# Optimization experiments

Hardware: AMD Instinct MI355X
Metric: run time of the kernel (lower is better)

## Reference

```python
import jax, jax.numpy as jnp
import numpy as np

B, N, M, K = 8, 9225, 4096, 32
D = 2          # coordinate dim
HID = 64       # MLP hidden
DOUT = 16      # MLP output / f_y channels


def setup_inputs() -> dict:
    key = jax.random.key(0)
    ks = jax.random.split(key, 10)
    y = jax.random.uniform(ks[0], (B, N, D), dtype=jnp.float32)
    x = jax.random.uniform(ks[1], (B, M, D), dtype=jnp.float32)
    f_y = jax.random.uniform(ks[2], (B, N, DOUT), dtype=jnp.float32)
    weights = jax.random.uniform(ks[3], (B, N), dtype=jnp.float32)
    neighbors_index = jax.random.randint(ks[4], (B, M, K), 0, N, dtype=jnp.int64)
    drop = jax.random.uniform(ks[5], (B, M, K)) < 0.1
    neighbors_index = jnp.where(drop, jnp.int64(-1), neighbors_index)
    # LinearChannelMLP params: 4 -> 64 -> 16, gelu between
    W1 = jax.random.normal(ks[6], (2 * D, HID), dtype=jnp.float32) * (1.0 / np.sqrt(2 * D))
    b1 = jnp.zeros((HID,), dtype=jnp.float32)
    W2 = jax.random.normal(ks[7], (HID, DOUT), dtype=jnp.float32) * (1.0 / np.sqrt(HID))
    b2 = jnp.zeros((DOUT,), dtype=jnp.float32)
    return {"y": y, "x": x, "f_y": f_y, "weights": weights,
            "W1": W1, "b1": b1, "W2": W2, "b2": b2,
            "neighbors_index": neighbors_index}


def _batched_gather(table, idx):
    # table: [B, N, ...], idx: [B, M, K] -> [B, M, K, ...]
    return jax.vmap(lambda t, i: t[i])(table, idx)


def reference(y, x, f_y, weights, W1, b1, W2, b2, neighbors_index):
    idx = jnp.where(neighbors_index == -1, 0, neighbors_index)      # [B,M,K]
    valid = (neighbors_index != -1).astype(y.dtype)[..., None]      # [B,M,K,1]

    rep_y = _batched_gather(y, idx)                                 # [B,M,K,D]
    in_f = _batched_gather(f_y, idx)                                # [B,M,K,DOUT]
    self_x = jnp.broadcast_to(x[:, :, None, :], rep_y.shape)        # [B,M,K,D]

    agg = jnp.concatenate([rep_y, self_x], axis=-1)                 # [B,M,K,2D]
    h = jax.nn.gelu(agg @ W1 + b1, approximate=False)               # [B,M,K,HID]
    kval = h @ W2 + b2                                              # [B,M,K,DOUT]

    kval = kval * in_f                                              # linear transform: k(x,y)*f(y)
    w_nbr = _batched_gather(weights, idx)[..., None]                # [B,M,K,1]
    kval = kval * w_nbr * valid
    return kval.sum(axis=2)                                         # [B,M,DOUT]
```

## Files before the change

### kernel.cpp

```cpp
#include <hip/hip_runtime.h>
#include <hip/hip_bf16.h>

#define B_    8
#define N_    9225
#define M_    4096
#define K_    32
#define HID_  64
#define DOUT_ 16

typedef __attribute__((ext_vector_type(8))) short short8;
typedef __attribute__((ext_vector_type(4))) float floatx4;
typedef __attribute__((ext_vector_type(2))) float f32x2;

static __device__ __forceinline__ short f2bf(float f) {
    __hip_bfloat16 h = __float2bfloat16(f);
    return __builtin_bit_cast(short, h);
}
static __device__ __forceinline__ f32x2 splat2(float v) { return (f32x2){v, v}; }
static __device__ __forceinline__ int bpermi(int src_bytes, int v) {
    return __builtin_amdgcn_ds_bpermute(src_bytes, v);
}
static __device__ __forceinline__ float bpermf(int src_bytes, float v) {
    return __builtin_bit_cast(float,
        __builtin_amdgcn_ds_bpermute(src_bytes, __builtin_bit_cast(int, v)));
}

static __device__ __forceinline__ float row16_sum(float v) {
    int t;
    t = __builtin_amdgcn_update_dpp(0, __builtin_bit_cast(int, v), 0x111, 0xF, 0xF, true);
    v += __builtin_bit_cast(float, t);
    t = __builtin_amdgcn_update_dpp(0, __builtin_bit_cast(int, v), 0x112, 0xF, 0xF, true);
    v += __builtin_bit_cast(float, t);
    t = __builtin_amdgcn_update_dpp(0, __builtin_bit_cast(int, v), 0x114, 0xF, 0xF, true);
    v += __builtin_bit_cast(float, t);
    t = __builtin_amdgcn_update_dpp(0, __builtin_bit_cast(int, v), 0x118, 0xF, 0xF, true);
    v += __builtin_bit_cast(float, t);
    return v;
}

static __device__ __forceinline__ f32x2 gelu2(f32x2 x) {
    const f32x2 xsq = x * x;
    const f32x2 t   = __builtin_elementwise_fma(xsq, splat2(0.035677408f), splat2(0.79788456f));
    const f32x2 z   = x * t;
    const f32x2 u   = z * z;
    const f32x2 a   = u + splat2(105.0f);
    const f32x2 nin = __builtin_elementwise_fma(u, a, splat2(945.0f));
    const f32x2 num = z * nin;
    const f32x2 bq  = __builtin_elementwise_fma(u, splat2(15.0f), splat2(420.0f));
    const f32x2 den = __builtin_elementwise_fma(u, bq, splat2(945.0f));
    const f32x2 r   = { __builtin_amdgcn_rcpf(den[0]), __builtin_amdgcn_rcpf(den[1]) };
    f32x2 th = num * r;
    th = __builtin_elementwise_min(__builtin_elementwise_max(th, splat2(-1.0f)), splat2(1.0f));
    const f32x2 hx = x * splat2(0.5f);
    return __builtin_elementwise_fma(hx, th, hx);
}

__global__ __launch_bounds__(256) void it_kernel(
    const float* __restrict__ y,
    const float* __restrict__ x,
    const float* __restrict__ f_y,
    const float* __restrict__ weights,
    const float* __restrict__ W1,
    const float* __restrict__ b1,
    const float* __restrict__ W2,
    const float* __restrict__ b2,
    const int*   __restrict__ nbr,
    float*       __restrict__ out)
{
    __shared__ float W1L[4][64];
    __shared__ float b1L[64];
    __shared__ float b2L[16];

    const int tid  = threadIdx.x;
    W1L[tid >> 6][tid & 63] = W1[tid];
    if (tid < 64) b1L[tid] = b1[tid];
    if (tid < 16) b2L[tid] = b2[tid];

    const int lane = tid & 63;
    const int q    = lane >> 4;
    const int nlo  = lane & 15;
    const int blk   = blockIdx.x;
    const int batch = blk & 7;
    const int pidx  = (blk >> 3) * 4 + (tid >> 6);
    const int row0  = __builtin_amdgcn_readfirstlane(batch * M_ + pidx * 2);
    const int bbase = batch * N_;

    const int r_g = lane >> 5, kk = lane & 31;
    const int raw = nbr[(size_t)(row0 + r_g) * K_ + kk];
    const int vld = raw >= 0;
    const int bn_g = bbase + (vld ? raw : 0);
    const float2 yvg = *(const float2*)(y + (size_t)bn_g * 2);
    const float  wg  = vld ? weights[bn_g] : 0.0f;

    short8 w2f[2];
    #pragma unroll
    for (int ch = 0; ch < 2; ++ch)
        #pragma unroll
        for (int jj = 0; jj < 8; ++jj)
            w2f[ch][jj] = f2bf(W2[(ch*32 + q*8 + jj) * DOUT_ + nlo]);

    __syncthreads();

    float partial[4] = {0.f, 0.f, 0.f, 0.f};
    #pragma unroll
    for (int ph = 0; ph < 4; ++ph) {
        const int it = ph >> 1, h = ph & 1;
        const int src = ((it << 5) + (h << 4) + nlo) << 2;

        const int bn = bpermi(src, bn_g);
        const floatx4 fv = *(const floatx4*)(f_y + (size_t)bn * 16 + q * 4);

        f32x2 yv;
        yv[0] = bpermf(src, yvg.x);
        yv[1] = bpermf(src, yvg.y);
        const float s = bpermf(src, wg);
        const float2 xv = *(const float2*)(x + (size_t)(row0 + it) * 2);

        short8 hf[2];
        #pragma unroll
        for (int ch = 0; ch < 2; ++ch) {
            #pragma unroll
            for (int p = 0; p < 4; ++p) {
                const int j = ch*32 + q*8 + 2*p;
                f32x2 hin = *(const f32x2*)&b1L[j];
                hin = __builtin_elementwise_fma(splat2(yv[0]), *(const f32x2*)&W1L[0][j], hin);
                hin = __builtin_elementwise_fma(splat2(yv[1]), *(const f32x2*)&W1L[1][j], hin);
                hin = __builtin_elementwise_fma(splat2(xv.x),  *(const f32x2*)&W1L[2][j], hin);
                hin = __builtin_elementwise_fma(splat2(xv.y),  *(const f32x2*)&W1L[3][j], hin);
                const f32x2 g = gelu2(hin);
                hf[ch][2*p]     = f2bf(g[0]);
                hf[ch][2*p + 1] = f2bf(g[1]);
            }
        }
        floatx4 acc = *(const floatx4*)&b2L[q*4];
        acc = __builtin_amdgcn_mfma_f32_16x16x32_bf16(w2f[0], hf[0], acc, 0, 0, 0);
        acc = __builtin_amdgcn_mfma_f32_16x16x32_bf16(w2f[1], hf[1], acc, 0, 0, 0);
        #pragma unroll
        for (int r4 = 0; r4 < 4; ++r4)
            partial[r4] = fmaf(acc[r4], fv[r4] * s, partial[r4]);

        if (h == 1) {
            #pragma unroll
            for (int r4 = 0; r4 < 4; ++r4)
                partial[r4] = row16_sum(partial[r4]);
            if (nlo == 15) {
                floatx4 o = {partial[0], partial[1], partial[2], partial[3]};
                *(floatx4*)(out + (size_t)(row0 + it) * DOUT_ + q*4) = o;
            }
            #pragma unroll
            for (int r4 = 0; r4 < 4; ++r4) partial[r4] = 0.f;
        }
    }
}

extern "C" void kernel_launch(void* const* d_in, const int* in_sizes, int n_in,
                              void* d_out, int out_size, void* d_ws, size_t ws_size,
                              hipStream_t stream) {
    const float* y   = (const float*)d_in[0];
    const float* x   = (const float*)d_in[1];
    const float* f_y = (const float*)d_in[2];
    const float* w   = (const float*)d_in[3];
    const float* W1  = (const float*)d_in[4];
    const float* b1  = (const float*)d_in[5];
    const float* W2  = (const float*)d_in[6];
    const float* b2  = (const float*)d_in[7];
    const int*   nbr = (const int*)d_in[8];
    float* out = (float*)d_out;

    dim3 grid(B_ * M_ / 8), block(256);
    hipLaunchKernelGGL(it_kernel, grid, block, 0, stream,
                       y, x, f_y, w, W1, b1, W2, b2, nbr, out);
}
```

Baseline: 106.1 us.

## Compute first MLP layer with bf16 MFMA instead of scalar FMAs from LDS

Replaces the per-lane scalar FMA evaluation of the 4->64 first layer (weights read from shared memory) with four 16x16x32 bf16 MFMAs. The inputs and a constant one for the bias are packed into the B fragment, and W1/b1 are held in registers. W2 fragments are reindexed to match the MFMA output layout. This also removes the shared-memory staging and the __syncthreads. In exchange the first-layer inputs and weights are rounded to bf16, which lowers precision, and most of each MFMA's K dimension is zero padding.

```diff
diff --git a/kernel.cpp b/kernel.cpp
--- a/kernel.cpp
+++ b/kernel.cpp
@@ -67,15 +67,7 @@
     const int*   __restrict__ nbr,
     float*       __restrict__ out)
 {
-    __shared__ float W1L[4][64];
-    __shared__ float b1L[64];
-    __shared__ float b2L[16];
-
     const int tid  = threadIdx.x;
-    W1L[tid >> 6][tid & 63] = W1[tid];
-    if (tid < 64) b1L[tid] = b1[tid];
-    if (tid < 16) b2L[tid] = b2[tid];
-
     const int lane = tid & 63;
     const int q    = lane >> 4;
     const int nlo  = lane & 15;
@@ -92,14 +84,30 @@
     const float2 yvg = *(const float2*)(y + (size_t)bn_g * 2);
     const float  wg  = vld ? weights[bn_g] : 0.0f;
 
+    short8 a1f[4];
+    #pragma unroll
+    for (int t = 0; t < 4; ++t) {
+        #pragma unroll
+        for (int jj = 0; jj < 8; ++jj) {
+            const int k = q * 8 + jj;
+            float v = 0.0f;
+            if (k < 4)       v = W1[k * 64 + t * 16 + nlo];
+            else if (k == 4) v = b1[t * 16 + nlo];
+            a1f[t][jj] = f2bf(v);
+        }
+    }
+
     short8 w2f[2];
     #pragma unroll
     for (int ch = 0; ch < 2; ++ch)
         #pragma unroll
-        for (int jj = 0; jj < 8; ++jj)
-            w2f[ch][jj] = f2bf(W2[(ch*32 + q*8 + jj) * DOUT_ + nlo]);
+        for (int jj = 0; jj < 8; ++jj) {
+            const int j = (ch * 2 + (jj >> 2)) * 16 + q * 4 + (jj & 3);
+            w2f[ch][jj] = f2bf(W2[j * DOUT_ + nlo]);
+        }
 
-    __syncthreads();
+    const floatx4 b2v = *(const floatx4*)(b2 + q * 4);
+    const short one_bf = f2bf(1.0f);
 
     float partial[4] = {0.f, 0.f, 0.f, 0.f};
     #pragma unroll
@@ -116,23 +124,37 @@
         const float s = bpermf(src, wg);
         const float2 xv = *(const float2*)(x + (size_t)(row0 + it) * 2);
 
+        short8 bfrag = {0, 0, 0, 0, 0, 0, 0, 0};
+        if (q == 0) {
+            bfrag[0] = f2bf(yv[0]);
+            bfrag[1] = f2bf(yv[1]);
+            bfrag[2] = f2bf(xv.x);
+            bfrag[3] = f2bf(xv.y);
+            bfrag[4] = one_bf;
+        }
+
+        floatx4 accT[4];
+        #pragma unroll
+        for (int t = 0; t < 4; ++t) {
+            floatx4 z4 = {0.f, 0.f, 0.f, 0.f};
+            accT[t] = __builtin_amdgcn_mfma_f32_16x16x32_bf16(a1f[t], bfrag, z4, 0, 0, 0);
+        }
+
         short8 hf[2];
         #pragma unroll
-        for (int ch = 0; ch < 2; ++ch) {
+        for (int ch = 0; ch < 2; ++ch)
             #pragma unroll
-            for (int p = 0; p < 4; ++p) {
-                const int j = ch*32 + q*8 + 2*p;
-                f32x2 hin = *(const f32x2*)&b1L[j];
-                hin = __builtin_elementwise_fma(splat2(yv[0]), *(const f32x2*)&W1L[0][j], hin);
-                hin = __builtin_elementwise_fma(splat2(yv[1]), *(const f32x2*)&W1L[1][j], hin);
-                hin = __builtin_elementwise_fma(splat2(xv.x),  *(const f32x2*)&W1L[2][j], hin);
-                hin = __builtin_elementwise_fma(splat2(xv.y),  *(const f32x2*)&W1L[3][j], hin);
-                const f32x2 g = gelu2(hin);
-                hf[ch][2*p]     = f2bf(g[0]);
-                hf[ch][2*p + 1] = f2bf(g[1]);
+            for (int half = 0; half < 2; ++half) {
+                const floatx4 a = accT[ch * 2 + half];
+                const f32x2 g0 = gelu2((f32x2){a[0], a[1]});
+                const f32x2 g1 = gelu2((f32x2){a[2], a[3]});
+                hf[ch][half * 4 + 0] = f2bf(g0[0]);
+                hf[ch][half * 4 + 1] = f2bf(g0[1]);
+                hf[ch][half * 4 + 2] = f2bf(g1[0]);
+                hf[ch][half * 4 + 3] = f2bf(g1[1]);
             }
-        }
-        floatx4 acc = *(const floatx4*)&b2L[q*4];
+
+        floatx4 acc = b2v;
         acc = __builtin_amdgcn_mfma_f32_16x16x32_bf16(w2f[0], hf[0], acc, 0, 0, 0);
         acc = __builtin_amdgcn_mfma_f32_16x16x32_bf16(w2f[1], hf[1], acc, 0, 0, 0);
         #pragma unroll
@@ -145,7 +167,7 @@
                 partial[r4] = row16_sum(partial[r4]);
             if (nlo == 15) {
                 floatx4 o = {partial[0], partial[1], partial[2], partial[3]};
-                *(floatx4*)(out + (size_t)(row0 + it) * DOUT_ + q*4) = o;
+                *(floatx4*)(out + (size_t)(row0 + it) * DOUT_ + q * 4) = o;
             }
             #pragma unroll
             for (int r4 = 0; r4 < 4; ++r4) partial[r4] = 0.f;
```

New measurement: 106.5 us. Within noise of the previous version (+0.4%).
